# Kernel tuning notes

Measured on AMD Instinct MI355X. Metric: run time of the kernel, lower is better.

The kernel has to match this reference:

```python
import jax, jax.numpy as jnp
import numpy as np

DIM = 256
NUM_HEADS = 8
HEAD_DIM = DIM // NUM_HEADS


def setup_inputs() -> dict:
    key = jax.random.key(0)
    k1, k2, k3, k4 = jax.random.split(key, 4)
    b, n = 4, 2048
    x = jax.random.normal(k1, (b, n, DIM), dtype=jnp.float32)
    # Linear weights with fan-in scaling (matches nn.Linear init magnitude,
    # keeps exp(qk) numerically sane since the original has no max-subtraction).
    Wqkv = jax.random.normal(k2, (DIM, 3 * DIM), dtype=jnp.float32) * (DIM ** -0.5)
    Wout = jax.random.normal(k3, (DIM, DIM), dtype=jnp.float32) * (DIM ** -0.5)
    bout = jax.random.normal(k4, (DIM,), dtype=jnp.float32) * 0.01
    return {"x": x, "Wqkv": Wqkv, "Wout": Wout, "bout": bout}


def reference(x, Wqkv, Wout, bout):
    b, n, d = x.shape
    h, hd = NUM_HEADS, HEAD_DIM
    scale = hd ** -0.5
    qkv = x @ Wqkv  # [b, n, 3d]
    q, k, v = jnp.split(qkv, 3, axis=-1)
    # [b, h, n, hd]
    q = q.reshape(b, n, h, hd).transpose(0, 2, 1, 3) * scale
    k = k.reshape(b, n, h, hd).transpose(0, 2, 1, 3)
    v = v.reshape(b, n, h, hd).transpose(0, 2, 1, 3)
    # Original KeOps path: unnormalized exp (no max-subtraction), separate
    # numerator / denominator reductions, eps in denominator.
    scores = jnp.einsum('bhnd,bhmd->bhnm', q, k)  # [b, h, n, n]
    e = jnp.exp(scores)
    denom = jnp.sum(e, axis=-1, keepdims=True)          # [b, h, n, 1]
    numer = jnp.einsum('bhnm,bhmd->bhnd', e, v)         # [b, h, n, hd]
    out = numer / (denom + 1e-6)
    out = out.transpose(0, 2, 1, 3).reshape(b, n, d)
    return out @ Wout + bout
```

## Files before the change

### kernel.cpp

```cpp
#include <hip/hip_runtime.h>

#define DIM 256
#define NHEADS 8
#define HDIM 32

typedef _Float16 half8_t __attribute__((ext_vector_type(8)));
typedef _Float16 half4_t __attribute__((ext_vector_type(4)));
typedef float float4_t __attribute__((ext_vector_type(4)));

__device__ __forceinline__ float fast_exp2(float x) {
#if __has_builtin(__builtin_amdgcn_exp2f)
    return __builtin_amdgcn_exp2f(x);
#else
    return __expf(x * 0.6931471805599453f);
#endif
}

__device__ __forceinline__ void gload_lds16(const void* g, void* l) {
    __builtin_amdgcn_global_load_lds((const __attribute__((address_space(1))) void*)g,
                                     (__attribute__((address_space(3))) void*)l,
                                     16, 0, 0);
}

__global__ __launch_bounds__(256) void prep(const float* __restrict__ x,
                                            const float* __restrict__ Wqkv,
                                            const float* __restrict__ Wout,
                                            _Float16* __restrict__ xh,
                                            _Float16* __restrict__ WqT,
                                            _Float16* __restrict__ WoT) {
    __shared__ float ts[32][33];
    const int bid = blockIdx.x, t = threadIdx.x;
    if (bid < 1024) {
        size_t idx = (size_t)bid * 2048 + (size_t)t * 8;
        float tmp[8];
        *reinterpret_cast<float4*>(tmp)     = *reinterpret_cast<const float4*>(x + idx);
        *reinterpret_cast<float4*>(tmp + 4) = *reinterpret_cast<const float4*>(x + idx + 4);
        half8_t h;
        #pragma unroll
        for (int j = 0; j < 8; ++j) h[j] = (_Float16)tmp[j];
        *reinterpret_cast<half8_t*>(xh + idx) = h;
    } else {
        const float* src; _Float16* dst; int K, N, kb, nb;
        if (bid < 1024 + 192) { int b2 = bid - 1024; src = Wqkv; dst = WqT; K = 256; N = 768; nb = b2 % 24; kb = b2 / 24; }
        else                  { int b3 = bid - 1216; src = Wout; dst = WoT; K = 256; N = 256; nb = b3 % 8;  kb = b3 / 8; }
        const int tx = t & 31, ty = t >> 5;
        #pragma unroll
        for (int i = 0; i < 4; ++i) {
            int k = kb * 32 + ty + i * 8;
            ts[ty + i * 8][tx] = src[(size_t)k * N + nb * 32 + tx];
        }
        __syncthreads();
        #pragma unroll
        for (int i = 0; i < 4; ++i) {
            int nl = ty + i * 8;
            dst[(size_t)(nb * 32 + nl) * K + kb * 32 + tx] = (_Float16)ts[tx][nl];
        }
    }
}

template <bool OUT_HALF, bool VSPLIT, int MROWS>
__global__ __launch_bounds__(256) void gemm_h(const _Float16* __restrict__ A,
                                              const _Float16* __restrict__ BT,
                                              const float* __restrict__ bias,
                                              void* __restrict__ Cv,
                                              _Float16* __restrict__ VTo,
                                              int M, int N, int K, int ldc) {
    constexpr int BM = MROWS * 32;
    __shared__ alignas(16) _Float16 As[BM * 32];
    __shared__ alignas(16) _Float16 Bs[128 * 32];
    const int t = threadIdx.x, lane = t & 63, wave = t >> 6;
    const int l16 = lane & 15, quad = lane >> 4;
    const int m0 = blockIdx.y * BM, n0 = blockIdx.x * 128;
    const int wr = (wave >> 1) * (MROWS * 16), wc = (wave & 1) * 64;
    constexpr float QS = 0.17677669529663687f * 1.4426950408889634f;
    float4_t acc[MROWS][4];
    #pragma unroll
    for (int i = 0; i < MROWS; ++i)
        #pragma unroll
        for (int j = 0; j < 4; ++j) acc[i][j] = (float4_t){0.f, 0.f, 0.f, 0.f};

    const int srow = lane >> 2;
    const int scol = (lane & 3) * 8;

    for (int k0 = 0; k0 < K; k0 += 32) {
        #pragma unroll
        for (int i = 0; i < MROWS / 2; ++i) {
            int chunk = i * 4 + wave;
            int r = chunk * 16 + srow;
            gload_lds16(A + (size_t)(m0 + r) * K + k0 + scol, As + chunk * 512);
        }
        #pragma unroll
        for (int i = 0; i < 2; ++i) {
            int chunk = i * 4 + wave;
            int r = chunk * 16 + srow;
            gload_lds16(BT + (size_t)(n0 + r) * K + k0 + scol, Bs + chunk * 512);
        }
        __syncthreads();
        half8_t af[MROWS], bf[4];
        #pragma unroll
        for (int i = 0; i < MROWS; ++i)
            af[i] = *reinterpret_cast<const half8_t*>(As + (wr + i * 16 + l16) * 32 + quad * 8);
        #pragma unroll
        for (int j = 0; j < 4; ++j)
            bf[j] = *reinterpret_cast<const half8_t*>(Bs + (wc + j * 16 + l16) * 32 + quad * 8);
        #pragma unroll
        for (int i = 0; i < MROWS; ++i)
            #pragma unroll
            for (int j = 0; j < 4; ++j)
                acc[i][j] = __builtin_amdgcn_mfma_f32_16x16x32_f16(af[i], bf[j], acc[i][j], 0, 0, 0);
        __syncthreads();
    }

    if (VSPLIT && n0 >= 512) {
        const int bb = m0 >> 11;
        const int tok0 = (m0 & 2047) + wr;
        #pragma unroll
        for (int i = 0; i < MROWS; ++i)
            #pragma unroll
            for (int j = 0; j < 4; ++j) {
                int vcol = n0 + wc + j * 16 + l16 - 512;
                int hh = vcol >> 5, d = vcol & 31;
                half4_t p;
                #pragma unroll
                for (int r = 0; r < 4; ++r) p[r] = (_Float16)acc[i][j][r];
                *reinterpret_cast<half4_t*>(
                    VTo + ((size_t)(bb * NHEADS + hh) * HDIM + d) * 2048
                        + tok0 + i * 16 + quad * 4) = p;
            }
    } else {
        float bv[4] = {0.f, 0.f, 0.f, 0.f};
        if (bias != nullptr) {
            #pragma unroll
            for (int j = 0; j < 4; ++j) bv[j] = bias[n0 + wc + j * 16 + l16];
        }
        #pragma unroll
        for (int i = 0; i < MROWS; ++i)
            #pragma unroll
            for (int r = 0; r < 4; ++r) {
                int row = m0 + wr + i * 16 + quad * 4 + r;
                #pragma unroll
                for (int j = 0; j < 4; ++j) {
                    int col = n0 + wc + j * 16 + l16;
                    float v = acc[i][j][r] + bv[j];
                    if (VSPLIT && n0 < 256) v *= QS;
                    if (OUT_HALF) ((_Float16*)Cv)[(size_t)row * ldc + col] = (_Float16)v;
                    else          ((float*)Cv)[(size_t)row * ldc + col] = v;
                }
            }
    }
}


#define LOADKV(P, k0)                                                              \
    do {                                                                           \
        const _Float16* kp_ = kbase + (size_t)(k0) * 512;                          \
        k##P##0 = *reinterpret_cast<const half8_t*>(kp_);                          \
        k##P##1 = *reinterpret_cast<const half8_t*>(kp_ + (size_t)16 * 512);       \
        k##P##2 = *reinterpret_cast<const half8_t*>(kp_ + (size_t)32 * 512);       \
        k##P##3 = *reinterpret_cast<const half8_t*>(kp_ + (size_t)48 * 512);       \
        const _Float16* vp_ = vbase + (k0);                                        \
        v##P##0 = *reinterpret_cast<const half8_t*>(vp_);                          \
        v##P##1 = *reinterpret_cast<const half8_t*>(vp_ + (size_t)16 * 2048);      \
        v##P##2 = *reinterpret_cast<const half8_t*>(vp_ + 32);                     \
        v##P##3 = *reinterpret_cast<const half8_t*>(vp_ + 32 + (size_t)16 * 2048); \
    } while (0)

#define EXPKB(KF, e0, e1)                                                          \
    do {                                                                           \
        float4_t st0 = __builtin_amdgcn_mfma_f32_16x16x32_f16(KF, qf0, z, 0, 0, 0);\
        float4_t st1 = __builtin_amdgcn_mfma_f32_16x16x32_f16(KF, qf1, z, 0, 0, 0);\
        auto lo0 = __builtin_amdgcn_cvt_pkrtz(fast_exp2(st0[0]), fast_exp2(st0[1]));\
        auto hi0 = __builtin_amdgcn_cvt_pkrtz(fast_exp2(st0[2]), fast_exp2(st0[3]));\
        e0 = (half4_t){(_Float16)lo0[0], (_Float16)lo0[1],                         \
                       (_Float16)hi0[0], (_Float16)hi0[1]};                        \
        auto lo1 = __builtin_amdgcn_cvt_pkrtz(fast_exp2(st1[0]), fast_exp2(st1[1]));\
        auto hi1 = __builtin_amdgcn_cvt_pkrtz(fast_exp2(st1[2]), fast_exp2(st1[3]));\
        e1 = (half4_t){(_Float16)lo1[0], (_Float16)lo1[1],                         \
                       (_Float16)hi1[0], (_Float16)hi1[1]};                        \
    } while (0)

#define PVCHUNK(ea0, ea1, eb0, eb1, VF0, VF1)                                      \
    do {                                                                           \
        *reinterpret_cast<half4_t*>(esw + l16 * 40 + quad * 4) = ea0;              \
        *reinterpret_cast<half4_t*>(esw + (16 + l16) * 40 + quad * 4) = ea1;       \
        *reinterpret_cast<half4_t*>(esw + l16 * 40 + 16 + quad * 4) = eb0;         \
        *reinterpret_cast<half4_t*>(esw + (16 + l16) * 40 + 16 + quad * 4) = eb1;  \
        half8_t ef0 = *reinterpret_cast<const half8_t*>(esw + l16 * 40 + quad * 8);\
        half8_t ef1 = *reinterpret_cast<const half8_t*>(esw + (16 + l16) * 40 + quad * 8);\
        num00 = __builtin_amdgcn_mfma_f32_16x16x32_f16(ef0, VF0, num00, 0, 0, 0);  \
        num01 = __builtin_amdgcn_mfma_f32_16x16x32_f16(ef0, VF1, num01, 0, 0, 0);  \
        dacc0 = __builtin_amdgcn_mfma_f32_16x16x32_f16(ef0, onef, dacc0, 0, 0, 0); \
        num10 = __builtin_amdgcn_mfma_f32_16x16x32_f16(ef1, VF0, num10, 0, 0, 0);  \
        num11 = __builtin_amdgcn_mfma_f32_16x16x32_f16(ef1, VF1, num11, 0, 0, 0);  \
        dacc1 = __builtin_amdgcn_mfma_f32_16x16x32_f16(ef1, onef, dacc1, 0, 0, 0); \
    } while (0)

#define STEP(P)                                                                    \
    do {                                                                           \
        half4_t e00, e01, e10, e11, e20, e21, e30, e31;                            \
        EXPKB(k##P##0, e00, e01);                                                  \
        EXPKB(k##P##1, e10, e11);                                                  \
        EXPKB(k##P##2, e20, e21);                                                  \
        EXPKB(k##P##3, e30, e31);                                                  \
        PVCHUNK(e00, e01, e10, e11, v##P##0, v##P##1);                             \
        PVCHUNK(e20, e21, e30, e31, v##P##2, v##P##3);                             \
    } while (0)

__global__ __launch_bounds__(256, 2) void attn_v8(const _Float16* __restrict__ qkh,
                                                  const _Float16* __restrict__ VT,
                                                  _Float16* __restrict__ attnh) {
    __shared__ alignas(16) _Float16 es[4][32][40];
    const int bid = blockIdx.x;
    const int qb = bid & 15;
    const int bh = bid >> 4;
    const int b = bh >> 3, h = bh & 7;
    const int t = threadIdx.x, lane = t & 63, wave = t >> 6;
    const int l16 = lane & 15, quad = lane >> 4;
    const int bN = b * 2048;
    const int q0w = qb * 128 + wave * 32;

    half8_t qf0, qf1;
    {
        const _Float16* qrow = qkh + (size_t)(bN + q0w + l16) * 512 + h * HDIM + quad * 8;
        qf0 = *reinterpret_cast<const half8_t*>(qrow);
        qf1 = *reinterpret_cast<const half8_t*>(qrow + (size_t)16 * 512);
    }

    const _Float16* kbase = qkh + (size_t)(bN + l16) * 512 + 256 + h * HDIM + quad * 8;
    const _Float16* vbase = VT + (size_t)bh * HDIM * 2048 + (size_t)l16 * 2048 + quad * 8;

    float4_t num00 = {0.f, 0.f, 0.f, 0.f}, num01 = {0.f, 0.f, 0.f, 0.f};
    float4_t num10 = {0.f, 0.f, 0.f, 0.f}, num11 = {0.f, 0.f, 0.f, 0.f};
    float4_t dacc0 = {0.f, 0.f, 0.f, 0.f}, dacc1 = {0.f, 0.f, 0.f, 0.f};

    half8_t onef;
    #pragma unroll
    for (int j = 0; j < 8; ++j) onef[j] = (_Float16)1.0f;

    _Float16* esw = &es[wave][0][0];
    const float4_t z = {0.f, 0.f, 0.f, 0.f};

    half8_t kA0, kA1, kA2, kA3, vA0, vA1, vA2, vA3;
    half8_t kB0, kB1, kB2, kB3, vB0, vB1, vB2, vB3;
    LOADKV(A, 0);
    #pragma unroll 2
    for (int k0 = 0; k0 < 2048; k0 += 128) {
        LOADKV(B, k0 + 64);
        STEP(A);
        if (k0 + 128 < 2048) LOADKV(A, k0 + 128);
        STEP(B);
    }

    _Float16* ob = attnh + (size_t)(bN + q0w) * DIM + h * HDIM;
    #pragma unroll
    for (int r = 0; r < 4; ++r) {
        float rcp0 = 1.0f / (dacc0[r] + 1e-6f);
        float rcp1 = 1.0f / (dacc1[r] + 1e-6f);
        size_t ro0 = (size_t)(quad * 4 + r) * DIM;
        size_t ro1 = (size_t)(16 + quad * 4 + r) * DIM;
        ob[ro0 + l16]      = (_Float16)(num00[r] * rcp0);
        ob[ro0 + 16 + l16] = (_Float16)(num01[r] * rcp0);
        ob[ro1 + l16]      = (_Float16)(num10[r] * rcp1);
        ob[ro1 + 16 + l16] = (_Float16)(num11[r] * rcp1);
    }
}

extern "C" void kernel_launch(void* const* d_in, const int* in_sizes, int n_in,
                              void* d_out, int out_size, void* d_ws, size_t ws_size,
                              hipStream_t stream) {
    const float* x    = (const float*)d_in[0];
    const float* Wqkv = (const float*)d_in[1];
    const float* Wout = (const float*)d_in[2];
    const float* bout = (const float*)d_in[3];
    float* out = (float*)d_out;
    const int M = 8192;

    _Float16* xh    = (_Float16*)d_ws;
    _Float16* WqT   = xh + (size_t)M * DIM;
    _Float16* WoT   = WqT + 768 * 256;
    _Float16* qkh   = WoT + 256 * 256;
    _Float16* vt    = qkh + (size_t)M * 512;
    _Float16* attnh = vt + (size_t)32 * HDIM * 2048;

    hipLaunchKernelGGL(prep, dim3(1280), dim3(256), 0, stream, x, Wqkv, Wout, xh, WqT, WoT);
    hipLaunchKernelGGL((gemm_h<true, true, 4>), dim3(6, 64), dim3(256), 0, stream,
                       xh, WqT, (const float*)nullptr, (void*)qkh, vt, M, 768, DIM, 512);
    hipLaunchKernelGGL(attn_v8, dim3(512), dim3(256), 0, stream, qkh, vt, attnh);
    hipLaunchKernelGGL((gemm_h<false, false, 2>), dim3(2, 128), dim3(256), 0, stream,
                       attnh, WoT, bout, (void*)out, (_Float16*)nullptr, M, DIM, DIM, DIM);
}
```

Before: 146.2 us.

## Split attention over key halves with separate combine kernel

Splits the key dimension into two halves so the attention kernel runs 1024 blocks instead of 512. Each block writes unnormalized fp16 partial numerators and fp32 denominators, and a new combine kernel sums the halves and normalizes. It also drops the double-buffered K/V register prefetch, raises the occupancy hint to 4 blocks per CU, swizzles the block order, and halves the QKV GEMM tile rows. This buys more parallelism and occupancy at the cost of an extra kernel launch, extra global traffic, and fp16 rounding of the unnormalized partial sums, which could overflow.

```diff
diff --git a/kernel.cpp b/kernel.cpp
--- a/kernel.cpp
+++ b/kernel.cpp
@@ -206,18 +206,21 @@
         PVCHUNK(e20, e21, e30, e31, v##P##2, v##P##3);                             \
     } while (0)
 
-__global__ __launch_bounds__(256, 2) void attn_v8(const _Float16* __restrict__ qkh,
+__global__ __launch_bounds__(256, 4) void attn_v9(const _Float16* __restrict__ qkh,
                                                   const _Float16* __restrict__ VT,
-                                                  _Float16* __restrict__ attnh) {
+                                                  _Float16* __restrict__ NUM,
+                                                  float* __restrict__ DEN) {
     __shared__ alignas(16) _Float16 es[4][32][40];
-    const int bid = blockIdx.x;
-    const int qb = bid & 15;
-    const int bh = bid >> 4;
+    const int bid = ((blockIdx.x & 7) << 7) | (blockIdx.x >> 3);
+    const int kh = bid & 1;
+    const int qb = (bid >> 1) & 15;
+    const int bh = bid >> 5;
     const int b = bh >> 3, h = bh & 7;
     const int t = threadIdx.x, lane = t & 63, wave = t >> 6;
     const int l16 = lane & 15, quad = lane >> 4;
     const int bN = b * 2048;
     const int q0w = qb * 128 + wave * 32;
+    const int kbeg = kh * 1024;
 
     half8_t qf0, qf1;
     {
@@ -241,28 +244,42 @@
     const float4_t z = {0.f, 0.f, 0.f, 0.f};
 
     half8_t kA0, kA1, kA2, kA3, vA0, vA1, vA2, vA3;
-    half8_t kB0, kB1, kB2, kB3, vB0, vB1, vB2, vB3;
-    LOADKV(A, 0);
-    #pragma unroll 2
-    for (int k0 = 0; k0 < 2048; k0 += 128) {
-        LOADKV(B, k0 + 64);
+    for (int k0 = kbeg; k0 < kbeg + 1024; k0 += 64) {
+        LOADKV(A, k0);
         STEP(A);
-        if (k0 + 128 < 2048) LOADKV(A, k0 + 128);
-        STEP(B);
-    }
-
-    _Float16* ob = attnh + (size_t)(bN + q0w) * DIM + h * HDIM;
+    }
+
+    _Float16* ob = NUM + (size_t)kh * 2097152 + (size_t)(bN + q0w) * DIM + h * HDIM;
     #pragma unroll
     for (int r = 0; r < 4; ++r) {
-        float rcp0 = 1.0f / (dacc0[r] + 1e-6f);
-        float rcp1 = 1.0f / (dacc1[r] + 1e-6f);
         size_t ro0 = (size_t)(quad * 4 + r) * DIM;
         size_t ro1 = (size_t)(16 + quad * 4 + r) * DIM;
-        ob[ro0 + l16]      = (_Float16)(num00[r] * rcp0);
-        ob[ro0 + 16 + l16] = (_Float16)(num01[r] * rcp0);
-        ob[ro1 + l16]      = (_Float16)(num10[r] * rcp1);
-        ob[ro1 + 16 + l16] = (_Float16)(num11[r] * rcp1);
-    }
+        ob[ro0 + l16]      = (_Float16)num00[r];
+        ob[ro0 + 16 + l16] = (_Float16)num01[r];
+        ob[ro1 + l16]      = (_Float16)num10[r];
+        ob[ro1 + 16 + l16] = (_Float16)num11[r];
+    }
+    if (l16 == 0) {
+        #pragma unroll
+        for (int r = 0; r < 4; ++r) {
+            DEN[kh * 65536 + bh * 2048 + q0w + quad * 4 + r]      = dacc0[r];
+            DEN[kh * 65536 + bh * 2048 + q0w + 16 + quad * 4 + r] = dacc1[r];
+        }
+    }
+}
+
+__global__ __launch_bounds__(256) void combine(const _Float16* __restrict__ NUM,
+                                               const float* __restrict__ DEN,
+                                               _Float16* __restrict__ attnh) {
+    const size_t idx = ((size_t)blockIdx.x * 256 + threadIdx.x) * 8;
+    const int row = (int)(idx >> 8);
+    const int c = (int)(idx & 255);
+    const int b = row >> 11, tok = row & 2047, h = c >> 5;
+    const int di = (b * 8 + h) * 2048 + tok;
+    float rcp = 1.0f / (DEN[di] + DEN[di + 65536] + 1e-6f);
+    half8_t n0 = *reinterpret_cast<const half8_t*>(NUM + idx);
+    half8_t n1 = *reinterpret_cast<const half8_t*>(NUM + idx + 2097152);
+    *reinterpret_cast<half8_t*>(attnh + idx) = (n0 + n1) * (_Float16)rcp;
 }
 
 extern "C" void kernel_launch(void* const* d_in, const int* in_sizes, int n_in,
@@ -280,12 +297,15 @@
     _Float16* WoT   = WqT + 768 * 256;
     _Float16* qkh   = WoT + 256 * 256;
     _Float16* vt    = qkh + (size_t)M * 512;
-    _Float16* attnh = vt + (size_t)32 * HDIM * 2048;
+    _Float16* NUM   = vt + (size_t)32 * HDIM * 2048;
+    float*    DEN   = (float*)(NUM + (size_t)2 * M * DIM);
+    _Float16* attnh = (_Float16*)(DEN + 2 * 65536);
 
     hipLaunchKernelGGL(prep, dim3(1280), dim3(256), 0, stream, x, Wqkv, Wout, xh, WqT, WoT);
-    hipLaunchKernelGGL((gemm_h<true, true, 4>), dim3(6, 64), dim3(256), 0, stream,
+    hipLaunchKernelGGL((gemm_h<true, true, 2>), dim3(6, 128), dim3(256), 0, stream,
                        xh, WqT, (const float*)nullptr, (void*)qkh, vt, M, 768, DIM, 512);
-    hipLaunchKernelGGL(attn_v8, dim3(512), dim3(256), 0, stream, qkh, vt, attnh);
+    hipLaunchKernelGGL(attn_v9, dim3(1024), dim3(256), 0, stream, qkh, vt, NUM, DEN);
+    hipLaunchKernelGGL(combine, dim3(1024), dim3(256), 0, stream, NUM, DEN, attnh);
     hipLaunchKernelGGL((gemm_h<false, false, 2>), dim3(2, 128), dim3(256), 0, stream,
                        attnh, WoT, bout, (void*)out, (_Float16*)nullptr, M, DIM, DIM, DIM);
 }
```

Measured after the change: 147.2 us. Within noise of the previous version (+0.7%).
